# Optimization experiments

Measured on AMD Instinct MI355X. Metric: run time of the kernel, lower is better.

Reference implementation:

```python
import jax, jax.numpy as jnp
import numpy as np

N_RAYS = 8192
N_SURF = 2048
EPS = 1e-18  # matches torch zero-denominator patch value


def setup_inputs() -> dict:
    key = jax.random.key(0)
    k1, k2, k3 = jax.random.split(key, 3)
    o = jax.random.normal(k1, (N_RAYS, 3), dtype=jnp.float32)
    d = jax.random.normal(k2, (N_RAYS, 3), dtype=jnp.float32)
    V = jax.random.normal(k3, (N_SURF, 4, 3), dtype=jnp.float32)
    return {"o": o, "d": d, "V": V}


def _safe(x):
    # torch code sets exact-zero denominators to 1e-18 via nonzero() indexing
    return jnp.where(x == 0.0, EPS, x)


def reference(o, d, V):
    # --- get_intersections: ray-plane intersection scalars t (N, M) ---
    v = jnp.cross(V[:, 1] - V[:, 0], V[:, 2] - V[:, 0])          # (M,3) plane normals
    v = v / jnp.linalg.norm(v, axis=1, keepdims=True)
    k = -jnp.sum(v * V[:, 3], axis=1)                             # (M,) plane offsets
    vo = o @ v.T                                                  # (N,M)
    vd = d @ v.T                                                  # (N,M)
    t = -(k[None, :] + vo) / vd                                   # (N,M)

    # intersection points r = o + t*d, broadcast over surfaces -> (N,M,3)
    r = o[:, None, :] + t[..., None] * d[:, None, :]

    # --- get_onsurface_surface_intersections: barycentric masking ---
    a = V[None, :, 0]  # (1,M,3) broadcast instead of .repeat
    b = V[None, :, 1]
    c = V[None, :, 2]
    ax, ay, az = a[..., 0], a[..., 1], a[..., 2]
    rx, ry, rz = r[..., 0], r[..., 1], r[..., 2]

    A = ax * rz - az * rx
    B = ax * b[..., 2] - az * b[..., 0]
    C = ax * ry - ay * rx
    D = ax * b[..., 1] - ay * b[..., 0]
    E = ax * c[..., 2] - az * c[..., 0]
    F = B * (ay * c[..., 0] - ax * c[..., 1])
    G = D

    gam = (G * (A * D - B * C)) / _safe(D * (E * G + F))          # (N,M)
    beta = (C + gam * (ay * c[..., 0] - ax * c[..., 1])) / _safe(D)
    alpha = (rx - (beta * b[..., 0] + gam * c[..., 0])) / _safe(ax)

    mask = (beta > 0.0) & (gam > 0.0) & (alpha > 0.0)             # (N,M) bool
    return t * mask.astype(t.dtype)                               # masked intersection depths
```

## Files before the change

kernel.cpp:

```cpp
#include <hip/hip_runtime.h>


#define N_RAYS 8192
#define N_SURF 2048
constexpr int RPB = 32;

__device__ __forceinline__ float safef(float x) {
    return (x == 0.0f) ? 1e-18f : x;
}

__global__ __launch_bounds__(256) void rt_kernel(
    const float* __restrict__ o, const float* __restrict__ dr,
    const float* __restrict__ V, float* __restrict__ out)
{
    const int s = blockIdx.x * 256 + threadIdx.x;

    const float4 p0 = *(const float4*)(V + (size_t)s * 12);
    const float4 p1 = *(const float4*)(V + (size_t)s * 12 + 4);
    const float4 p2 = *(const float4*)(V + (size_t)s * 12 + 8);
    const float ax = p0.x, ay = p0.y, az = p0.z;
    const float bx = p0.w, by = p1.x, bz = p1.y;
    const float cx = p1.z, cy = p1.w, cz = p2.x;
    const float wx = p2.y, wy = p2.z, wz = p2.w;

    const float e0x = bx - ax, e0y = by - ay, e0z = bz - az;
    const float e1x = cx - ax, e1y = cy - ay, e1z = cz - az;
    const float nx = e0y * e1z - e0z * e1y;
    const float ny = e0z * e1x - e0x * e1z;
    const float nz = e0x * e1y - e0y * e1x;
    const float nrm = sqrtf(nx * nx + ny * ny + nz * nz);
    const float vx = nx / nrm, vy = ny / nrm, vz = nz / nrm;
    const float k = -(vx * wx + vy * wy + vz * wz);

    const float B  = ax * bz - az * bx;
    const float D  = ax * by - ay * bx;
    const float E  = ax * cz - az * cx;
    const float P  = ay * cx - ax * cy;
    const float F  = B * P;
    const float den_g = safef(D * (E * D + F));
    const float sD    = safef(D);
    const float sAX   = safef(ax);

    const float DB = D * B, DD = D * D;
    const float g0 = (DB * ay - DD * az) / den_g;
    const float g1 = -(DB * ax) / den_g;
    const float g2 = (DD * ax) / den_g;
    const float b0 = -ay / sD;
    const float b1 = ax / sD;
    const float bp = P / sD;
    const float a0 = 1.0f / sAX;
    const float ab = -bx / sAX;
    const float ac = -cx / sAX;

    const int ray0 = blockIdx.y * RPB;
    float* outp = out + (size_t)ray0 * N_SURF + s;
#pragma unroll 4
    for (int i = 0; i < RPB; ++i) {
        const int ray = ray0 + i;
        const float o0 = o[ray * 3 + 0], o1 = o[ray * 3 + 1], o2 = o[ray * 3 + 2];
        const float d0 = dr[ray * 3 + 0], d1 = dr[ray * 3 + 1], d2 = dr[ray * 3 + 2];

        const float vo = fmaf(o0, vx, fmaf(o1, vy, o2 * vz));
        const float vd = fmaf(d0, vx, fmaf(d1, vy, d2 * vz));
        const float t  = (-(k + vo)) / vd;

        const float rx = fmaf(t, d0, o0);
        const float ry = fmaf(t, d1, o1);
        const float rz = fmaf(t, d2, o2);

        const float gam   = fmaf(g0, rx, fmaf(g1, ry, g2 * rz));
        const float beta  = fmaf(b0, rx, fmaf(b1, ry, bp * gam));
        const float alpha = fmaf(a0, rx, fmaf(ab, beta, ac * gam));

        const float m = (beta > 0.0f && gam > 0.0f && alpha > 0.0f) ? 1.0f : 0.0f;
        outp[(size_t)i * N_SURF] = t * m;
    }
}

extern "C" void kernel_launch(void* const* d_in, const int* in_sizes, int n_in,
                              void* d_out, int out_size, void* d_ws, size_t ws_size,
                              hipStream_t stream) {
    const float* o  = (const float*)d_in[0];
    const float* dr = (const float*)d_in[1];
    const float* V  = (const float*)d_in[2];
    float* out = (float*)d_out;

    dim3 grid(N_SURF / 256, N_RAYS / RPB);
    rt_kernel<<<grid, dim3(256), 0, stream>>>(o, dr, V, out);
}
```

Baseline: 93.43 us.

## Precompute per-surface coefficients in separate kernel and simplify per-ray math

Splits per-surface coefficient setup into a precompute kernel that writes 16 floats per surface to workspace, and the trace kernel loads them instead of recomputing them in every block. Folds beta and alpha into direct linear forms of the hit point, replaces the division with a hardware reciprocal, and uses a min-based mask. It also raises unroll to 8. The cost is an extra kernel launch, and the approximate reciprocal plus reassociated coefficients can change rounding and flip borderline mask decisions.

```diff
diff --git a/kernel.cpp b/kernel.cpp
--- a/kernel.cpp
+++ b/kernel.cpp
@@ -9,12 +9,10 @@
     return (x == 0.0f) ? 1e-18f : x;
 }
 
-__global__ __launch_bounds__(256) void rt_kernel(
-    const float* __restrict__ o, const float* __restrict__ dr,
-    const float* __restrict__ V, float* __restrict__ out)
+__device__ __forceinline__ void surface_coeffs(
+    const float* __restrict__ V, int s,
+    float4& c0, float4& c1, float4& c2, float4& c3)
 {
-    const int s = blockIdx.x * 256 + threadIdx.x;
-
     const float4 p0 = *(const float4*)(V + (size_t)s * 12);
     const float4 p1 = *(const float4*)(V + (size_t)s * 12 + 4);
     const float4 p2 = *(const float4*)(V + (size_t)s * 12 + 8);
@@ -45,35 +43,68 @@
     const float g0 = (DB * ay - DD * az) / den_g;
     const float g1 = -(DB * ax) / den_g;
     const float g2 = (DD * ax) / den_g;
-    const float b0 = -ay / sD;
-    const float b1 = ax / sD;
-    const float bp = P / sD;
-    const float a0 = 1.0f / sAX;
-    const float ab = -bx / sAX;
-    const float ac = -cx / sAX;
+    const float b0 = -ay / sD, b1 = ax / sD, bp = P / sD;
+    const float bb0 = b0 + bp * g0;
+    const float bb1 = b1 + bp * g1;
+    const float bb2 = bp * g2;
+    const float a0 = 1.0f / sAX, ab = -bx / sAX, ac = -cx / sAX;
+    const float aa0 = a0 + ab * bb0 + ac * g0;
+    const float aa1 = ab * bb1 + ac * g1;
+    const float aa2 = ab * bb2 + ac * g2;
+
+    c0 = make_float4(vx, vy, vz, k);
+    c1 = make_float4(g0, g1, g2, 0.0f);
+    c2 = make_float4(bb0, bb1, bb2, 0.0f);
+    c3 = make_float4(aa0, aa1, aa2, 0.0f);
+}
+
+__global__ __launch_bounds__(256) void precompute_kernel(
+    const float* __restrict__ V, float* __restrict__ C)
+{
+    const int s = blockIdx.x * 256 + threadIdx.x;
+    float4 c0, c1, c2, c3;
+    surface_coeffs(V, s, c0, c1, c2, c3);
+    float4* c4 = (float4*)(C + (size_t)s * 16);
+    c4[0] = c0; c4[1] = c1; c4[2] = c2; c4[3] = c3;
+}
+
+template <bool FUSED>
+__global__ __launch_bounds__(256) void trace_kernel(
+    const float* __restrict__ o, const float* __restrict__ dr,
+    const float* __restrict__ VorC, float* __restrict__ out)
+{
+    const int s = blockIdx.x * 256 + threadIdx.x;
+
+    float4 c0, c1, c2, c3;
+    if constexpr (FUSED) {
+        surface_coeffs(VorC, s, c0, c1, c2, c3);
+    } else {
+        const float4* c4 = (const float4*)(VorC + (size_t)s * 16);
+        c0 = c4[0]; c1 = c4[1]; c2 = c4[2]; c3 = c4[3];
+    }
 
     const int ray0 = blockIdx.y * RPB;
     float* outp = out + (size_t)ray0 * N_SURF + s;
-#pragma unroll 4
+#pragma unroll 8
     for (int i = 0; i < RPB; ++i) {
         const int ray = ray0 + i;
         const float o0 = o[ray * 3 + 0], o1 = o[ray * 3 + 1], o2 = o[ray * 3 + 2];
         const float d0 = dr[ray * 3 + 0], d1 = dr[ray * 3 + 1], d2 = dr[ray * 3 + 2];
 
-        const float vo = fmaf(o0, vx, fmaf(o1, vy, o2 * vz));
-        const float vd = fmaf(d0, vx, fmaf(d1, vy, d2 * vz));
-        const float t  = (-(k + vo)) / vd;
+        const float vo_k = fmaf(o0, c0.x, fmaf(o1, c0.y, fmaf(o2, c0.z, c0.w)));
+        const float vd   = fmaf(d0, c0.x, fmaf(d1, c0.y, d2 * c0.z));
+        const float t    = -vo_k * __builtin_amdgcn_rcpf(vd);
 
         const float rx = fmaf(t, d0, o0);
         const float ry = fmaf(t, d1, o1);
         const float rz = fmaf(t, d2, o2);
 
-        const float gam   = fmaf(g0, rx, fmaf(g1, ry, g2 * rz));
-        const float beta  = fmaf(b0, rx, fmaf(b1, ry, bp * gam));
-        const float alpha = fmaf(a0, rx, fmaf(ab, beta, ac * gam));
+        const float gam   = fmaf(c1.x, rx, fmaf(c1.y, ry, c1.z * rz));
+        const float beta  = fmaf(c2.x, rx, fmaf(c2.y, ry, c2.z * rz));
+        const float alpha = fmaf(c3.x, rx, fmaf(c3.y, ry, c3.z * rz));
 
-        const float m = (beta > 0.0f && gam > 0.0f && alpha > 0.0f) ? 1.0f : 0.0f;
-        outp[(size_t)i * N_SURF] = t * m;
+        const float mn = fminf(fminf(beta, gam), alpha);
+        outp[(size_t)i * N_SURF] = (mn > 0.0f) ? t : 0.0f;
     }
 }
 
@@ -85,6 +116,14 @@
     const float* V  = (const float*)d_in[2];
     float* out = (float*)d_out;
 
+    const size_t coeff_bytes = (size_t)N_SURF * 16 * sizeof(float);
     dim3 grid(N_SURF / 256, N_RAYS / RPB);
-    rt_kernel<<<grid, dim3(256), 0, stream>>>(o, dr, V, out);
+
+    if (ws_size >= coeff_bytes) {
+        float* C = (float*)d_ws;
+        precompute_kernel<<<dim3(N_SURF / 256), dim3(256), 0, stream>>>(V, C);
+        trace_kernel<false><<<grid, dim3(256), 0, stream>>>(o, dr, C, out);
+    } else {
+        trace_kernel<true><<<grid, dim3(256), 0, stream>>>(o, dr, V, out);
+    }
 }
```

New measurement: 86.93 us. 1.07x faster.
